# Performance work log

Hardware: AMD Instinct MI355X
Metric: run time of the kernel (lower is better)

The kernel has to match this reference:

```python
import jax, jax.numpy as jnp
import numpy as np

SCALE = 64.0   # CosFace scale s
MARGIN = 0.35  # CosFace margin m
EPS = 1e-12


def setup_inputs() -> dict:
    key = jax.random.key(0)
    k1, k2, k3 = jax.random.split(key, 3)
    batch, feat_dim, num_classes = 512, 512, 100000
    return {
        "input": jax.random.normal(k1, (batch, feat_dim), dtype=jnp.float32),
        "label": jax.random.randint(k2, (batch,), 0, num_classes, dtype=jnp.int64),
        "w": jax.random.normal(k3, (feat_dim, num_classes), dtype=jnp.float32),
    }


def reference(input, label, w):
    # L2-normalize features (rows) and class weights (columns), as in _forward_train
    feat_norm = jnp.clip(jnp.linalg.norm(input, axis=1, keepdims=True), EPS, None)
    normed_feat = input / feat_norm                      # [B, D]
    w_norm = jnp.clip(jnp.linalg.norm(w, axis=0, keepdims=True), EPS, None)
    normed_w = w / w_norm                                # [D, C]
    cosine = jnp.clip(normed_feat @ normed_w, -1.0, 1.0)  # [B, C]
    # CosFace margin applied at the true-label position (get_probs_i)
    onehot = jax.nn.one_hot(label, w.shape[1], dtype=cosine.dtype)
    logits = SCALE * (cosine - MARGIN * onehot)          # [B, C]
    # loss = mean(logsumexp over all (sharded) classes - logit at true label)
    lse = jax.nn.logsumexp(logits, axis=1)               # [B]
    x = jnp.take_along_axis(logits, label[:, None], axis=1)[:, 0]  # [B]
    return jnp.mean(lse - x)
```

## Files before the change

### kernel.cpp

```cpp
#include <hip/hip_runtime.h>
#include <hip/hip_bf16.h>
#include <math.h>

#define BDIM 512
#define DDIM 512
#define CDIM 100000
#define NC 64
#define BK 64
#define NSLICE (DDIM / BK)
#define NCHUNK ((CDIM + NC - 1) / NC)

typedef __attribute__((ext_vector_type(8))) short short8;
typedef __attribute__((ext_vector_type(4))) float f32x4;

__device__ __forceinline__ unsigned short f2bf(float f) {
  unsigned int u = __builtin_bit_cast(unsigned int, f);
  u = (u + 0x7FFFu + ((u >> 16) & 1u)) >> 16;
  return (unsigned short)u;
}

__device__ __forceinline__ void gl_lds16(const unsigned short* g, unsigned short* l) {
  __builtin_amdgcn_global_load_lds(
      (const __attribute__((address_space(1))) void*)g,
      (__attribute__((address_space(3))) void*)l, 16, 0, 0);
}

__global__ void k_rownorm(const float* __restrict__ x, unsigned short* __restrict__ a) {
  const int b = blockIdx.x;
  const int tid = threadIdx.x;
  const float* row = x + (size_t)b * DDIM;
  float v0 = row[tid], v1 = row[tid + 256];
  float ss = v0 * v0 + v1 * v1;
  #pragma unroll
  for (int m = 1; m < 64; m <<= 1) ss += __shfl_xor(ss, m);
  __shared__ float sred[4];
  __shared__ float sinv;
  if ((tid & 63) == 0) sred[tid >> 6] = ss;
  __syncthreads();
  if (tid == 0) {
    float s = sred[0] + sred[1] + sred[2] + sred[3];
    sinv = 1.f / fmaxf(sqrtf(s), 1e-12f);
  }
  __syncthreads();
  const float inv = sinv;
  a[(size_t)b * DDIM + tid] = f2bf(v0 * inv);
  a[(size_t)b * DDIM + tid + 256] = f2bf(v1 * inv);
}

__global__ __launch_bounds__(512)
void k_main(const unsigned short* __restrict__ a,
            const float* __restrict__ w,
            const long long* __restrict__ label,
            float2* __restrict__ part,
            float* __restrict__ labellogit) {
  __shared__ __align__(16) unsigned short alds[2][DDIM * BK];
  __shared__ __align__(16) unsigned short blds[2][NC * BK];
  __shared__ float ssred[32][NC];
  __shared__ float invwn_sh[NC];

  const int t = threadIdx.x;
  const int chunk = blockIdx.x;
  const int c0 = chunk * NC;
  const bool tailblk = (c0 + NC > CDIM);

  const int wave = t >> 6;
  const int lane = t & 63;
  const int lhi = lane >> 4;
  const int llo = lane & 15;

  const int arsub  = lane >> 3;
  const int apiece = (lane & 7) ^ (lane >> 3);

  const int dgh = (t & 127) >> 2;
  const int bcg = ((t >> 7) << 2) | (t & 3);
  const int bc4 = bcg * 4;

  float4 p0, p1;
  float ssp0 = 0.f, ssp1 = 0.f, ssp2 = 0.f, ssp3 = 0.f;

  auto issueA = [&](int s) {
    #pragma unroll
    for (int i = 0; i < 8; i++) {
      const int r = i * 8 + wave;
      const int row = r * 8 + arsub;
      gl_lds16(a + (size_t)row * DDIM + s * BK + apiece * 8,
               &alds[s & 1][r * 512]);
    }
  };
  auto issueW = [&](int s) {
    const size_t base = (size_t)(s * BK + 2 * dgh) * CDIM + c0 + bc4;
    if (!tailblk) {
      p0 = *reinterpret_cast<const float4*>(w + base);
      p1 = *reinterpret_cast<const float4*>(w + base + CDIM);
    } else {
      #pragma unroll
      for (int j = 0; j < 4; j++) {
        const bool v = (c0 + bc4 + j) < CDIM;
        p0[j] = v ? w[base + j] : 0.f;
        p1[j] = v ? w[base + CDIM + j] : 0.f;
      }
    }
  };
  auto commitW = [&](int s) {
    ssp0 += p0.x * p0.x + p1.x * p1.x;
    ssp1 += p0.y * p0.y + p1.y * p1.y;
    ssp2 += p0.z * p0.z + p1.z * p1.z;
    ssp3 += p0.w * p0.w + p1.w * p1.w;
    unsigned int* b32 = reinterpret_cast<unsigned int*>(&blds[s & 1][0]);
    #pragma unroll
    for (int j = 0; j < 4; j++) {
      const int c = bc4 + j;
      const unsigned int pk = (unsigned int)f2bf(p0[j]) | ((unsigned int)f2bf(p1[j]) << 16);
      b32[c * 32 + (dgh ^ ((c & 7) << 2))] = pk;
    }
  };

  f32x4 acc[4][4];
  #pragma unroll
  for (int i = 0; i < 4; i++)
    #pragma unroll
    for (int j = 0; j < 4; j++)
      acc[i][j] = (f32x4){0.f, 0.f, 0.f, 0.f};

  issueA(0);
  issueW(0);

  for (int s = 0; s < NSLICE; s++) {
    asm volatile("s_waitcnt vmcnt(0)" ::: "memory");
    commitW(s);
    asm volatile("s_waitcnt lgkmcnt(0)" ::: "memory");
    __builtin_amdgcn_s_barrier();
    if (s + 1 < NSLICE) { issueA(s + 1); issueW(s + 1); }
    __builtin_amdgcn_sched_barrier(0);

    #pragma unroll
    for (int half = 0; half < 2; half++) {
      short8 af[4], bfr[4];
      #pragma unroll
      for (int rf = 0; rf < 4; rf++) {
        const int row = wave * 64 + rf * 16 + llo;
        af[rf] = *reinterpret_cast<const short8*>(
            &alds[s & 1][row * BK + ((((half << 2) + lhi) ^ (llo & 7)) << 3)]);
      }
      const int kloc = half * 32 + (lhi << 3);
      #pragma unroll
      for (int cf = 0; cf < 4; cf++) {
        const int c = cf * 16 + llo;
        bfr[cf] = *reinterpret_cast<const short8*>(
            &blds[s & 1][c * BK + (kloc ^ ((c & 7) << 3))]);
      }
      #pragma unroll
      for (int rf = 0; rf < 4; rf++)
        #pragma unroll
        for (int cf = 0; cf < 4; cf++)
          acc[rf][cf] = __builtin_amdgcn_mfma_f32_16x16x32_bf16(af[rf], bfr[cf], acc[rf][cf], 0, 0, 0);
    }
  }

  #pragma unroll
  for (int j = 0; j < 4; j++) {
    const float sv = (j == 0) ? ssp0 : (j == 1) ? ssp1 : (j == 2) ? ssp2 : ssp3;
    ssred[dgh][bc4 + j] = sv;
  }
  __syncthreads();
  if (t < NC) {
    float s = 0.f;
    #pragma unroll
    for (int i = 0; i < 32; i++) s += ssred[i][t];
    invwn_sh[t] = 1.f / fmaxf(sqrtf(s), 1e-12f);
  }
  __syncthreads();

  #pragma unroll
  for (int rf = 0; rf < 4; rf++) {
    #pragma unroll
    for (int r = 0; r < 4; r++) {
      const int row = wave * 64 + rf * 16 + (lhi << 2) + r;
      const int lab = (int)label[row];
      float vals[4];
      float mloc = -INFINITY;
      #pragma unroll
      for (int cf = 0; cf < 4; cf++) {
        const int cg = c0 + cf * 16 + llo;
        float cs = acc[rf][cf][r] * invwn_sh[cf * 16 + llo];
        cs = fminf(fmaxf(cs, -1.f), 1.f);
        float lg = 64.f * cs;
        if (cg == lab) { lg = 64.f * (cs - 0.35f); labellogit[row] = lg; }
        if (cg >= CDIM) lg = -INFINITY;
        vals[cf] = lg;
        mloc = fmaxf(mloc, lg);
      }
      float m = mloc;
      #pragma unroll
      for (int msk = 1; msk < 16; msk <<= 1) m = fmaxf(m, __shfl_xor(m, msk));
      float s = 0.f;
      #pragma unroll
      for (int cf = 0; cf < 4; cf++) s += __expf(vals[cf] - m);
      #pragma unroll
      for (int msk = 1; msk < 16; msk <<= 1) s += __shfl_xor(s, msk);
      if (llo == 0) part[(size_t)chunk * BDIM + row] = make_float2(m, s);
    }
  }
}

__global__ void k_rowreduce(const float2* __restrict__ part,
                            const float* __restrict__ labellogit,
                            float* __restrict__ rowloss) {
  const int row = blockIdx.x;
  const int tid = threadIdx.x;
  float m = -INFINITY, s = 0.f;
  for (int ch = tid; ch < NCHUNK; ch += 256) {
    float2 p = part[(size_t)ch * BDIM + row];
    float nm = fmaxf(m, p.x);
    s = s * __expf(m - nm) + p.y * __expf(p.x - nm);
    m = nm;
  }
  #pragma unroll
  for (int msk = 1; msk < 64; msk <<= 1) {
    float om = __shfl_xor(m, msk), os = __shfl_xor(s, msk);
    float nm = fmaxf(m, om);
    s = s * __expf(m - nm) + os * __expf(om - nm);
    m = nm;
  }
  __shared__ float sm[4], ssum[4];
  const int wv = tid >> 6, ln = tid & 63;
  if (ln == 0) { sm[wv] = m; ssum[wv] = s; }
  __syncthreads();
  if (tid == 0) {
    float M = sm[0], S = ssum[0];
    #pragma unroll
    for (int i = 1; i < 4; i++) {
      float nm = fmaxf(M, sm[i]);
      S = S * __expf(M - nm) + ssum[i] * __expf(sm[i] - nm);
      M = nm;
    }
    rowloss[row] = M + logf(S) - labellogit[row];
  }
}

__global__ void k_mean(const float* __restrict__ rowloss, float* __restrict__ out) {
  const int tid = threadIdx.x;
  float v = rowloss[tid];
  #pragma unroll
  for (int msk = 1; msk < 64; msk <<= 1) v += __shfl_xor(v, msk);
  __shared__ float sred[8];
  if ((tid & 63) == 0) sred[tid >> 6] = v;
  __syncthreads();
  if (tid == 0) {
    float s = 0.f;
    #pragma unroll
    for (int i = 0; i < 8; i++) s += sred[i];
    out[0] = s / (float)BDIM;
  }
}

extern "C" void kernel_launch(void* const* d_in, const int* in_sizes, int n_in,
                              void* d_out, int out_size, void* d_ws, size_t ws_size,
                              hipStream_t stream) {
  const float* input = (const float*)d_in[0];
  const long long* label = (const long long*)d_in[1];
  const float* w = (const float*)d_in[2];
  float* out = (float*)d_out;

  char* ws = (char*)d_ws;
  unsigned short* a_bf16 = (unsigned short*)ws;
  float2* part = (float2*)(ws + 512 * 1024);
  float* labellogit = (float*)(ws + 512 * 1024 + (size_t)BDIM * NCHUNK * sizeof(float2));
  float* rowloss = labellogit + BDIM;

  k_rownorm<<<BDIM, 256, 0, stream>>>(input, a_bf16);
  k_main<<<NCHUNK, 512, 0, stream>>>(a_bf16, w, label, part, labellogit);
  k_rowreduce<<<BDIM, 256, 0, stream>>>(part, labellogit, rowloss);
  k_mean<<<1, BDIM, 0, stream>>>(rowloss, out);
}
```

Baseline: 176.7 us.

## Load A fragments directly from global memory, drop A LDS staging

Removes the 512x64 bf16 A tile staged in LDS (64KB per buffer, two buffers) and has each wave read its MFMA A fragments straight from global/L2, since every block reuses the same small normalized feature matrix. The W pipeline is restructured to commit the next slice after the MFMAs, with a single barrier per slice and a fully unrolled loop. The column sum-of-squares reduction moves from a 32-row LDS pass to wave shuffles plus a small 8-row LDS table. The much smaller LDS footprint allows more blocks per CU. The cost is that A global loads now sit directly in front of the MFMAs and are only hidden by occupancy and cache hits.

Result: slower. 221.1 us (+25.1%).

```diff
diff --git a/kernel.cpp b/kernel.cpp
--- a/kernel.cpp
+++ b/kernel.cpp
@@ -19,12 +19,6 @@
   return (unsigned short)u;
 }
 
-__device__ __forceinline__ void gl_lds16(const unsigned short* g, unsigned short* l) {
-  __builtin_amdgcn_global_load_lds(
-      (const __attribute__((address_space(1))) void*)g,
-      (__attribute__((address_space(3))) void*)l, 16, 0, 0);
-}
-
 __global__ void k_rownorm(const float* __restrict__ x, unsigned short* __restrict__ a) {
   const int b = blockIdx.x;
   const int tid = threadIdx.x;
@@ -53,9 +47,8 @@
             const long long* __restrict__ label,
             float2* __restrict__ part,
             float* __restrict__ labellogit) {
-  __shared__ __align__(16) unsigned short alds[2][DDIM * BK];
   __shared__ __align__(16) unsigned short blds[2][NC * BK];
-  __shared__ float ssred[32][NC];
+  __shared__ float ssred[8][NC];
   __shared__ float invwn_sh[NC];
 
   const int t = threadIdx.x;
@@ -68,25 +61,12 @@
   const int lhi = lane >> 4;
   const int llo = lane & 15;
 
-  const int arsub  = lane >> 3;
-  const int apiece = (lane & 7) ^ (lane >> 3);
-
   const int dgh = (t & 127) >> 2;
-  const int bcg = ((t >> 7) << 2) | (t & 3);
-  const int bc4 = bcg * 4;
+  const int bc4 = (((t >> 7) << 2) | (t & 3)) * 4;
 
   float4 p0, p1;
   float ssp0 = 0.f, ssp1 = 0.f, ssp2 = 0.f, ssp3 = 0.f;
 
-  auto issueA = [&](int s) {
-    #pragma unroll
-    for (int i = 0; i < 8; i++) {
-      const int r = i * 8 + wave;
-      const int row = r * 8 + arsub;
-      gl_lds16(a + (size_t)row * DDIM + s * BK + apiece * 8,
-               &alds[s & 1][r * 512]);
-    }
-  };
   auto issueW = [&](int s) {
     const size_t base = (size_t)(s * BK + 2 * dgh) * CDIM + c0 + bc4;
     if (!tailblk) {
@@ -101,12 +81,12 @@
       }
     }
   };
-  auto commitW = [&](int s) {
+  auto commitW = [&](int buf) {
     ssp0 += p0.x * p0.x + p1.x * p1.x;
     ssp1 += p0.y * p0.y + p1.y * p1.y;
     ssp2 += p0.z * p0.z + p1.z * p1.z;
     ssp3 += p0.w * p0.w + p1.w * p1.w;
-    unsigned int* b32 = reinterpret_cast<unsigned int*>(&blds[s & 1][0]);
+    unsigned int* b32 = reinterpret_cast<unsigned int*>(&blds[buf][0]);
     #pragma unroll
     for (int j = 0; j < 4; j++) {
       const int c = bc4 + j;
@@ -122,26 +102,27 @@
     for (int j = 0; j < 4; j++)
       acc[i][j] = (f32x4){0.f, 0.f, 0.f, 0.f};
 
-  issueA(0);
+  const unsigned short* ab0 = a + (size_t)(wave * 64 + 0 * 16 + llo) * DDIM + (lhi << 3);
+  const unsigned short* ab1 = a + (size_t)(wave * 64 + 1 * 16 + llo) * DDIM + (lhi << 3);
+  const unsigned short* ab2 = a + (size_t)(wave * 64 + 2 * 16 + llo) * DDIM + (lhi << 3);
+  const unsigned short* ab3 = a + (size_t)(wave * 64 + 3 * 16 + llo) * DDIM + (lhi << 3);
+
   issueW(0);
-
+  commitW(0);
+  __syncthreads();
+
+  #pragma unroll
   for (int s = 0; s < NSLICE; s++) {
-    asm volatile("s_waitcnt vmcnt(0)" ::: "memory");
-    commitW(s);
-    asm volatile("s_waitcnt lgkmcnt(0)" ::: "memory");
-    __builtin_amdgcn_s_barrier();
-    if (s + 1 < NSLICE) { issueA(s + 1); issueW(s + 1); }
-    __builtin_amdgcn_sched_barrier(0);
+    if (s + 1 < NSLICE) issueW(s + 1);
 
     #pragma unroll
     for (int half = 0; half < 2; half++) {
+      const int koff = (s * 2 + half) * 32;
       short8 af[4], bfr[4];
-      #pragma unroll
-      for (int rf = 0; rf < 4; rf++) {
-        const int row = wave * 64 + rf * 16 + llo;
-        af[rf] = *reinterpret_cast<const short8*>(
-            &alds[s & 1][row * BK + ((((half << 2) + lhi) ^ (llo & 7)) << 3)]);
-      }
+      af[0] = *reinterpret_cast<const short8*>(ab0 + koff);
+      af[1] = *reinterpret_cast<const short8*>(ab1 + koff);
+      af[2] = *reinterpret_cast<const short8*>(ab2 + koff);
+      af[3] = *reinterpret_cast<const short8*>(ab3 + koff);
       const int kloc = half * 32 + (lhi << 3);
       #pragma unroll
       for (int cf = 0; cf < 4; cf++) {
@@ -155,18 +136,28 @@
         for (int cf = 0; cf < 4; cf++)
           acc[rf][cf] = __builtin_amdgcn_mfma_f32_16x16x32_bf16(af[rf], bfr[cf], acc[rf][cf], 0, 0, 0);
     }
-  }
-
-  #pragma unroll
-  for (int j = 0; j < 4; j++) {
-    const float sv = (j == 0) ? ssp0 : (j == 1) ? ssp1 : (j == 2) ? ssp2 : ssp3;
-    ssred[dgh][bc4 + j] = sv;
+
+    if (s + 1 < NSLICE) commitW((s + 1) & 1);
+    __syncthreads();
+  }
+
+  #pragma unroll
+  for (int msk = 4; msk < 64; msk <<= 1) {
+    ssp0 += __shfl_xor(ssp0, msk);
+    ssp1 += __shfl_xor(ssp1, msk);
+    ssp2 += __shfl_xor(ssp2, msk);
+    ssp3 += __shfl_xor(ssp3, msk);
+  }
+  if (lane < 4) {
+    ssred[wave][bc4 + 0] = ssp0;
+    ssred[wave][bc4 + 1] = ssp1;
+    ssred[wave][bc4 + 2] = ssp2;
+    ssred[wave][bc4 + 3] = ssp3;
   }
   __syncthreads();
   if (t < NC) {
-    float s = 0.f;
-    #pragma unroll
-    for (int i = 0; i < 32; i++) s += ssred[i][t];
+    const int p = t >> 4;
+    const float s = ssred[2 * p][t] + ssred[2 * p + 1][t];
     invwn_sh[t] = 1.f / fmaxf(sqrtf(s), 1e-12f);
   }
   __syncthreads();
```
